# Performance work log

Measured on AMD Instinct MI355X. Metric: run time of the kernel, lower is better.

Reference implementation:

```python
import jax, jax.numpy as jnp
import numpy as np

C = 128        # dim_in = dim_out = dim_mid (exp_ratio=1.0)
HEADS = 4      # C // dim_head
DH = 32        # dim_head
WS = 7         # window_size
EPS = 1e-6
SCALE = DH ** -0.5


def bn3d(x, g, b):
    # BatchNorm3d forward (training-mode batch stats), eps=1e-6
    m = jnp.mean(x, axis=(0, 2, 3, 4), keepdims=True)
    v = jnp.mean((x - m) ** 2, axis=(0, 2, 3, 4), keepdims=True)
    xn = (x - m) * jax.lax.rsqrt(v + EPS)
    return xn * g.reshape(1, -1, 1, 1, 1) + b.reshape(1, -1, 1, 1, 1)


def conv1x1(x, w):
    # 1x1x1 conv, no bias: w is (out, in)
    return jnp.einsum('oi,bihwd->bohwd', w, x)


def setup_inputs() -> dict:
    key = jax.random.key(0)
    ks = jax.random.split(key, 6)
    x = jax.random.normal(ks[0], (4, C, 28, 28, 28), jnp.float32)
    g_in = jnp.ones((C,), jnp.float32)
    b_in = jnp.zeros((C,), jnp.float32)
    w_qk = jax.random.normal(ks[1], (2 * C, C), jnp.float32) * (C ** -0.5)
    w_v = jax.random.normal(ks[2], (C, C), jnp.float32) * (C ** -0.5)
    w_cl = jax.random.normal(ks[3], (C, C, 3, 3, 3), jnp.float32) * ((C * 27) ** -0.5)
    g_cl = jnp.ones((C,), jnp.float32)
    b_cl = jnp.zeros((C,), jnp.float32)
    w_proj = jax.random.normal(ks[4], (C, C), jnp.float32) * (C ** -0.5)
    return {"x": x, "g_in": g_in, "b_in": b_in, "w_qk": w_qk, "w_v": w_v,
            "w_cl": w_cl, "g_cl": g_cl, "b_cl": b_cl, "w_proj": w_proj}


def reference(x, g_in, b_in, w_qk, w_v, w_cl, g_cl, b_cl, w_proj):
    B, Cc, H, W, D = x.shape
    shortcut = x
    x = bn3d(x, g_in, b_in)

    # strided window partition: einops '(h1 n1)' => h1 (window) is the OUTER factor
    n1, n2, n3 = H // WS, W // WS, D // WS  # chosen divisible -> zero pad
    xw = x.reshape(B, Cc, WS, n1, WS, n2, WS, n3)
    xw = xw.transpose(0, 3, 5, 7, 1, 2, 4, 6).reshape(B * n1 * n2 * n3, Cc, WS, WS, WS)
    b = xw.shape[0]
    L = WS ** 3

    # qk: 1x1 conv -> split q,k -> (b, heads, L, dh)
    qk = conv1x1(xw, w_qk).reshape(b, 2, HEADS, DH, L)
    q = qk[:, 0].transpose(0, 1, 3, 2)       # b h L d
    k = qk[:, 1]                             # b h d L
    attn = jax.nn.softmax(jnp.einsum('bhld,bhdm->bhlm', q, k) * SCALE, axis=-1)

    # v: 1x1 conv + relu (attn_pre=False)
    v = jax.nn.relu(conv1x1(xw, w_v)).reshape(b, HEADS, DH, L)  # b h d L
    xs = jnp.einsum('bhlm,bhdm->bhld', attn, v)                 # b h L d
    xs = xs.transpose(0, 1, 3, 2).reshape(b, Cc, WS, WS, WS)

    # reverse window partition
    x = xs.reshape(B, n1, n2, n3, Cc, WS, WS, WS)
    x = x.transpose(0, 4, 5, 1, 6, 2, 7, 3).reshape(B, Cc, H, W, D)

    # local 3x3x3 conv + BN + SiLU, residual (has_skip inside iRMB branch)
    y = jax.lax.conv_general_dilated(
        x, w_cl, window_strides=(1, 1, 1),
        padding=[(1, 1), (1, 1), (1, 1)],
        dimension_numbers=('NCDHW', 'OIDHW', 'NCDHW'))
    y = jax.nn.silu(bn3d(y, g_cl, b_cl))
    x = x + y  # SE is Identity (se_ratio=0)

    x = conv1x1(x, w_proj)
    return shortcut + x
```

## Files before the change

### kernel.cpp

```cpp
#include <hip/hip_runtime.h>
#include <hip/hip_bf16.h>

#define C      128
#define SP     21952
#define PT     87808
#define LW     343
#define EPS_   1e-6f
#define SCALE_ 0.17677669529663687f

#define MISC_A   0
#define MISC_B   128
#define MISC_BQK 256
#define MISC_BV  512
#define MISC_SUM 640
#define MISC_SQ  768
#define MISC_A2  896
#define MISC_B2  1024
#define MISC_XS  1152
#define MISC_XQ  1280

typedef __attribute__((ext_vector_type(8))) short bf16x8;
typedef __attribute__((ext_vector_type(4))) float f32x4;

__device__ __forceinline__ float b2f(unsigned short u){
  return __uint_as_float(((unsigned int)u) << 16);
}
__device__ __forceinline__ unsigned short f2b(float f){
  unsigned int u = __float_as_uint(f);
  u += 0x7fffu + ((u >> 16) & 1u);
  return (unsigned short)(u >> 16);
}

__global__ __launch_bounds__(256) void k0_partial(const float* __restrict__ x,
                                                  float* __restrict__ misc){
  int c = blockIdx.x & 127, chunk = blockIdx.x >> 7;
  int bb = chunk >> 1, half = chunk & 1;
  const float4* p = reinterpret_cast<const float4*>(
      x + (size_t)(bb*C + c)*SP + half*10976);
  int t = threadIdx.x;
  float s = 0.f, ss = 0.f;
  for (int i = t; i < 2744; i += 256){
    float4 v = p[i];
    s  += v.x + v.y + v.z + v.w;
    ss += v.x*v.x + v.y*v.y + v.z*v.z + v.w*v.w;
  }
  #pragma unroll
  for (int off = 32; off > 0; off >>= 1){
    s  += __shfl_xor(s,  off);
    ss += __shfl_xor(ss, off);
  }
  __shared__ float red[8];
  int wid = t >> 6, lane = t & 63;
  if (lane == 0){ red[wid] = s; red[4+wid] = ss; }
  __syncthreads();
  if (t == 0){
    atomicAdd(&misc[MISC_XS + c], red[0]+red[1]+red[2]+red[3]);
    atomicAdd(&misc[MISC_XQ + c], red[4]+red[5]+red[6]+red[7]);
  }
}

__global__ void k1_bias(const float* __restrict__ wqk, const float* __restrict__ wvv,
                        const float* __restrict__ gin, const float* __restrict__ bin,
                        float* __restrict__ misc){
  __shared__ float bv[128];
  int t = threadIdx.x;
  {
    float mean = misc[MISC_XS + t] / (float)PT;
    float var  = misc[MISC_XQ + t] / (float)PT - mean*mean;
    float a = rsqrtf(var + EPS_) * gin[t];
    float bb = bin[t] - mean * a;
    bv[t] = bb;
    if (blockIdx.x == 0){ misc[MISC_A + t] = a; misc[MISC_B + t] = bb; }
  }
  __syncthreads();
  int o = blockIdx.x*128 + t;
  float acc = 0.f;
  if (o < 256){
    const float* wr = wqk + (size_t)o*128;
    for (int c = 0; c < 128; ++c) acc += wr[c]*bv[c];
    misc[MISC_BQK + o] = acc;
  } else {
    const float* wr = wvv + (size_t)(o-256)*128;
    for (int c = 0; c < 128; ++c) acc += wr[c]*bv[c];
    misc[MISC_BV + (o-256)] = acc;
  }
}

__global__ void k1w(const float* __restrict__ wqk, const float* __restrict__ wvv,
                    unsigned short* __restrict__ w2){
  int idx = blockIdx.x*256 + threadIdx.x;
  int o = idx >> 7;
  float w = (o < 256) ? wqk[idx] : wvv[idx - 32768];
  unsigned short h = f2b(w);
  w2[idx] = h;
  w2[49152 + idx] = f2b(w - b2f(h));
}

__global__ __launch_bounds__(256) void k2_qkv(const float* __restrict__ x,
        const unsigned short* __restrict__ w2, const float* __restrict__ misc,
        unsigned short* __restrict__ qg, unsigned short* __restrict__ kg,
        unsigned short* __restrict__ vg){
  __shared__ __align__(16) unsigned short xh[8192];
  __shared__ __align__(16) unsigned short xl[8192];
  __shared__ float ascale[128];
  __shared__ unsigned int posTab[64];
  int t = threadIdx.x;
  int P0 = blockIdx.x * 64;
  int b = P0 / SP, sp0 = P0 % SP;
  if (t < 128) ascale[t] = misc[MISC_A + t];
  if (t < 64){
    int sp = sp0 + t;
    int h_ = sp / 784, rem = sp % 784;
    int w_ = rem / 28, d_ = rem % 28;
    int w1 = h_ & 3, s1 = h_ >> 2;
    int w2i = w_ & 3, s2 = w_ >> 2;
    int w3 = d_ & 3, s3 = d_ >> 2;
    int bw = ((b*4 + w1)*4 + w2i)*4 + w3;
    int l  = (s1*7 + s2)*7 + s3;
    posTab[t] = (unsigned int)(bw*43904 + l*32);
  }
  __syncthreads();
  {
    int p = t & 63;
    int ob = t >> 6;
    const float* xb = x + (size_t)b*C*SP + sp0 + p;
    for (int it = 0; it < 4; ++it){
      int c0 = (ob + it*4) * 8;
      unsigned int ph[4], pl[4];
      #pragma unroll
      for (int j = 0; j < 4; ++j){
        float f0 = xb[(size_t)(c0 + 2*j)*SP]     * ascale[c0 + 2*j];
        float f1 = xb[(size_t)(c0 + 2*j + 1)*SP] * ascale[c0 + 2*j + 1];
        unsigned short h0 = f2b(f0), h1 = f2b(f1);
        unsigned short l0 = f2b(f0 - b2f(h0)), l1 = f2b(f1 - b2f(h1));
        ph[j] = (unsigned int)h0 | ((unsigned int)h1 << 16);
        pl[j] = (unsigned int)l0 | ((unsigned int)l1 << 16);
      }
      int byte = (p*256 + c0*2) ^ ((p & 7) << 4);
      *reinterpret_cast<uint4*>((char*)xh + byte) = make_uint4(ph[0],ph[1],ph[2],ph[3]);
      *reinterpret_cast<uint4*>((char*)xl + byte) = make_uint4(pl[0],pl[1],pl[2],pl[3]);
    }
  }
  __syncthreads();
  int wid = t >> 6, lane = t & 63;
  int g = lane >> 4, ln = lane & 15;
  int wstart = wid * 96;
  f32x4 acc[6][4];
  #pragma unroll
  for (int nt = 0; nt < 6; ++nt){
    float bv = misc[256 + wstart + nt*16 + ln];
    #pragma unroll
    for (int mt = 0; mt < 4; ++mt) acc[nt][mt] = (f32x4){bv,bv,bv,bv};
  }
  #pragma unroll 1
  for (int kk = 0; kk < 4; ++kk){
    bf16x8 ah[4], al[4];
    #pragma unroll
    for (int mt = 0; mt < 4; ++mt){
      int row = mt*16 + ln;
      int byte = (row*256 + kk*64 + g*16) ^ ((ln & 7) << 4);
      ah[mt] = *reinterpret_cast<const bf16x8*>((const char*)xh + byte);
      al[mt] = *reinterpret_cast<const bf16x8*>((const char*)xl + byte);
    }
    #pragma unroll
    for (int nt = 0; nt < 6; ++nt){
      int o = wstart + nt*16 + ln;
      const unsigned short* wp = w2 + (size_t)o*128 + kk*32 + g*8;
      bf16x8 whf = *reinterpret_cast<const bf16x8*>(wp);
      bf16x8 wlf = *reinterpret_cast<const bf16x8*>(wp + 49152);
      #pragma unroll
      for (int mt = 0; mt < 4; ++mt){
        acc[nt][mt] = __builtin_amdgcn_mfma_f32_16x16x32_bf16(ah[mt], whf, acc[nt][mt], 0, 0, 0);
        acc[nt][mt] = __builtin_amdgcn_mfma_f32_16x16x32_bf16(al[mt], whf, acc[nt][mt], 0, 0, 0);
        acc[nt][mt] = __builtin_amdgcn_mfma_f32_16x16x32_bf16(ah[mt], wlf, acc[nt][mt], 0, 0, 0);
      }
    }
  }
  unsigned int ptab[16];
  #pragma unroll
  for (int mt = 0; mt < 4; ++mt)
    #pragma unroll
    for (int r = 0; r < 4; ++r)
      ptab[mt*4+r] = posTab[mt*16 + g*4 + r];
  #pragma unroll
  for (int nt = 0; nt < 6; ++nt){
    int o = wstart + nt*16 + ln;
    bool isv = (o >= 256);
    int oo = o & 127;
    unsigned short* dst = ((o < 128) ? qg : (o < 256 ? kg : vg)) + (oo >> 5)*10976 + (oo & 31);
    #pragma unroll
    for (int mt = 0; mt < 4; ++mt){
      #pragma unroll
      for (int r = 0; r < 4; ++r){
        float v = acc[nt][mt][r];
        if (isv) v = fmaxf(v, 0.f);
        dst[ptab[mt*4+r]] = f2b(v);
      }
    }
  }
}

__global__ __launch_bounds__(256) void k3_attn(const unsigned short* __restrict__ qg,
        const unsigned short* __restrict__ kg, const unsigned short* __restrict__ vg,
        unsigned short* __restrict__ xatt){
  __shared__ __align__(16) unsigned short klds[352*32];
  __shared__ __align__(16) unsigned short vper[32*360];
  __shared__ __align__(16) unsigned short pbuf[4][640];
  int bh = blockIdx.x;
  int bw = bh >> 2, h = bh & 3;
  int t = threadIdx.x;
  int wid = t >> 6, lane = t & 63;
  int g = lane >> 4, ln = lane & 15;
  const unsigned short* kbase = kg + (size_t)bh*LW*32;
  const unsigned short* vbase = vg + (size_t)bh*LW*32;
  const unsigned short* qbase = qg + (size_t)bh*LW*32;
  {
    const uint4* src = reinterpret_cast<const uint4*>(kbase);
    uint4* dst = reinterpret_cast<uint4*>(klds);
    for (int i = t; i < 1372; i += 256) dst[i] = src[i];
    for (int i = t; i < 288; i += 256) klds[10976 + i] = 0;
  }
  for (int idx = t; idx < 10976; idx += 256){
    int m = idx >> 5, d = idx & 31;
    int km = m & 31;
    int pk = ((km & 15) << 1) | (km >> 4);
    vper[d*360 + ((m >> 5) << 5) + pk] = vbase[idx];
  }
  for (int i = t; i < 288; i += 256){
    int m = 343 + (i >> 5), d = i & 31;
    int km = m & 31;
    int pk = ((km & 15) << 1) | (km >> 4);
    vper[d*360 + 320 + pk] = 0;
  }
  __syncthreads();
  int w1 = (bw>>4)&3, w2 = (bw>>2)&3, w3 = bw&3, b = bw>>6;
  unsigned short* pb = pbuf[wid];
  const f32x4 zero4 = {0.f, 0.f, 0.f, 0.f};
  for (int rt = wid; rt < 22; rt += 4){
    int row0 = rt << 4;
    bf16x8 qf = *reinterpret_cast<const bf16x8*>(qbase + (size_t)(row0 + ln)*32 + g*8);
    f32x4 s[22];
    #pragma unroll
    for (int nt = 0; nt < 22; ++nt){
      bf16x8 kf = *reinterpret_cast<const bf16x8*>(&klds[(nt*16 + ln)*32 + g*8]);
      s[nt] = __builtin_amdgcn_mfma_f32_16x16x32_bf16(qf, kf, zero4, 0, 0, 0);
    }
    float mxs[4];
    #pragma unroll
    for (int q = 0; q < 4; ++q){
      float m0 = -1e30f;
      #pragma unroll
      for (int nt = 0; nt < 21; ++nt) m0 = fmaxf(m0, s[nt][q]);
      if (ln < 7) m0 = fmaxf(m0, s[21][q]);
      #pragma unroll
      for (int off = 8; off > 0; off >>= 1) m0 = fmaxf(m0, __shfl_xor(m0, off));
      mxs[q] = m0 * SCALE_;
    }
    f32x4 o0 = zero4, o1 = zero4;
    float sums[4] = {0.f, 0.f, 0.f, 0.f};
    #pragma unroll
    for (int c = 0; c < 11; ++c){
      #pragma unroll
      for (int q = 0; q < 4; ++q){
        float e0 = __expf(fmaf(s[2*c][q],   SCALE_, -mxs[q]));
        float e1 = (c*32 + 16 + ln < 343)
                 ? __expf(fmaf(s[2*c+1][q], SCALE_, -mxs[q])) : 0.f;
        sums[q] += e0 + e1;
        unsigned int pkd;
        asm volatile("v_cvt_pk_bf16_f32 %0, %1, %2" : "=v"(pkd) : "v"(e0), "v"(e1));
        *reinterpret_cast<unsigned int*>(&pb[(g*4+q)*40 + (ln<<1)]) = pkd;
      }
      asm volatile("s_waitcnt lgkmcnt(0)" ::: "memory");
      __builtin_amdgcn_sched_barrier(0);
      bf16x8 pa  = *reinterpret_cast<const bf16x8*>(&pb[ln*40 + g*8]);
      bf16x8 vb0 = *reinterpret_cast<const bf16x8*>(&vper[ln*360       + (c<<5) + g*8]);
      bf16x8 vb1 = *reinterpret_cast<const bf16x8*>(&vper[(16+ln)*360  + (c<<5) + g*8]);
      o0 = __builtin_amdgcn_mfma_f32_16x16x32_bf16(pa, vb0, o0, 0, 0, 0);
      o1 = __builtin_amdgcn_mfma_f32_16x16x32_bf16(pa, vb1, o1, 0, 0, 0);
    }
    float iss[4];
    #pragma unroll
    for (int q = 0; q < 4; ++q){
      float sq = sums[q];
      #pragma unroll
      for (int off = 8; off > 0; off >>= 1) sq += __shfl_xor(sq, off);
      iss[q] = 1.f / sq;
    }
    #pragma unroll
    for (int q = 0; q < 4; ++q){
      int l = row0 + g*4 + q;
      if (l < 343){
        int ss1 = l/49, ss2 = (l/7)%7, ss3 = l%7;
        int sp = (ss1*4+w1)*784 + (ss2*4+w2)*28 + (ss3*4+w3);
        size_t gaddr = ((size_t)b*SP + sp)*128 + h*32;
        xatt[gaddr + ln]      = f2b(o0[q]*iss[q]);
        xatt[gaddr + 16 + ln] = f2b(o1[q]*iss[q]);
      }
    }
  }
}

__global__ void k_wprep(const float* __restrict__ wcl, unsigned short* __restrict__ wbf){
  int f = blockIdx.x*256 + threadIdx.x;
  int j  = f & 7;
  int oc = (f >> 3) & 127;
  int kgr= (f >> 10) & 7;
  int sl = f >> 13;
  int h  = sl / 27, tap = sl % 27;
  int ic = h*64 + kgr*8 + j;
  wbf[f] = f2b(wcl[((size_t)oc*128 + ic)*27 + tap]);
}

__global__ void k6w(const float* __restrict__ wproj, unsigned short* __restrict__ w6){
  int idx = blockIdx.x*256 + threadIdx.x;
  float w = wproj[idx];
  unsigned short h = f2b(w);
  w6[idx] = h;
  w6[16384 + idx] = f2b(w - b2f(h));
}

__global__ __launch_bounds__(256) void k4_mfma(const unsigned short* __restrict__ xag,
        const unsigned short* __restrict__ wbf, unsigned short* __restrict__ yg){
  __shared__ __align__(16) unsigned short halo[8*216*8];
  __shared__ __align__(16) unsigned short wt[2][8192];
  int t = threadIdx.x, wid = t >> 6, lane = t & 63;
  int stile = blockIdx.x;
  int b = stile / 343, srem = stile % 343;
  int z0 = (srem/49)*4, y0 = ((srem/7)%7)*4, x0 = (srem%7)*4;
  int mhalf = wid & 1, ohalf = wid >> 1;
  int nn = lane & 15, quad = lane >> 4;
  int mA = mhalf*32 + nn;
  int mB = mA + 16;
  int hp0 = (mA>>4)*36 + ((mA>>2)&3)*6 + (mA&3);
  int hp1 = (mB>>4)*36 + ((mB>>2)&3)*6 + (mB&3);
  f32x4 acc[2][4] = {};

  #define WLOAD(s_, buf_) do { \
    const unsigned short* gs = wbf + (size_t)(s_)*8192 + (size_t)(wid*4*64 + lane)*8; \
    _Pragma("unroll") \
    for (int it = 0; it < 4; ++it){ \
      __builtin_amdgcn_global_load_lds( \
        (const __attribute__((address_space(1))) unsigned int*)(gs + it*512), \
        (__attribute__((address_space(3))) unsigned int*)(&wt[buf_][(wid*4+it)*512]), \
        16, 0, 0); \
    } \
  } while(0)

  int s = 0;
  WLOAD(0, 0);
  for (int h = 0; h < 2; ++h){
    for (int cidx = t; cidx < 1728; cidx += 256){
      int kgr = cidx / 216, pos = cidx % 216;
      int uz = pos / 36, r36 = pos % 36, uy = r36 / 6, ux = r36 % 6;
      int zz = z0 - 1 + uz, yy = y0 - 1 + uy, xx = x0 - 1 + ux;
      uint4 v = make_uint4(0u,0u,0u,0u);
      if (zz >= 0 && zz < 28 && yy >= 0 && yy < 28 && xx >= 0 && xx < 28)
        v = *reinterpret_cast<const uint4*>(
              &xag[(((size_t)b*SP) + zz*784 + yy*28 + xx)*128 + h*64 + kgr*8]);
      *reinterpret_cast<uint4*>(&halo[(size_t)cidx*8]) = v;
    }
    __syncthreads();
    for (int tap = 0; tap < 27; ++tap){
      if (s + 1 < 54) WLOAD(s + 1, (s + 1) & 1);
      const unsigned short* wc = wt[s & 1];
      int dz = tap / 9, r9 = tap % 9, dy = r9 / 3, dx = r9 % 3;
      int off = dz*36 + dy*6 + dx;
      #pragma unroll
      for (int ks = 0; ks < 2; ++ks){
        int ksel = ks*4 + quad;
        bf16x8 a0 = *reinterpret_cast<const bf16x8*>(&halo[(ksel*216 + hp0 + off)*8]);
        bf16x8 a1 = *reinterpret_cast<const bf16x8*>(&halo[(ksel*216 + hp1 + off)*8]);
        #pragma unroll
        for (int nt = 0; nt < 4; ++nt){
          bf16x8 bb = *reinterpret_cast<const bf16x8*>(&wc[(ksel*128 + ohalf*64 + nt*16 + nn)*8]);
          acc[0][nt] = __builtin_amdgcn_mfma_f32_16x16x32_bf16(a0, bb, acc[0][nt], 0, 0, 0);
          acc[1][nt] = __builtin_amdgcn_mfma_f32_16x16x32_bf16(a1, bb, acc[1][nt], 0, 0, 0);
        }
      }
      ++s;
      __syncthreads();
    }
  }
  #pragma unroll
  for (int mt = 0; mt < 2; ++mt){
    #pragma unroll
    for (int nt = 0; nt < 4; ++nt){
      #pragma unroll
      for (int r = 0; r < 4; ++r){
        int m = mhalf*32 + mt*16 + quad*4 + r;
        int oc = ohalf*64 + nt*16 + nn;
        int pos = (z0 + (m>>4))*784 + (y0 + ((m>>2)&3))*28 + (x0 + (m&3));
        yg[((size_t)b*SP + pos)*128 + oc] = f2b(acc[mt][nt][r]);
      }
    }
  }
  #undef WLOAD
}

__global__ void k5_ystats(const unsigned short* __restrict__ yg, float* __restrict__ misc){
  int t = threadIdx.x;
  float s = 0.f, ss = 0.f;
  size_t base = (size_t)blockIdx.x * 32768 + t;
  for (int k = 0; k < 128; ++k){
    float v = b2f(yg[base + (size_t)k*256]);
    s += v; ss += v*v;
  }
  __shared__ float rs[256], rq[256];
  rs[t] = s; rq[t] = ss;
  __syncthreads();
  if (t < 128){
    atomicAdd(&misc[MISC_SUM + t], rs[t] + rs[t+128]);
    atomicAdd(&misc[MISC_SQ  + t], rq[t] + rq[t+128]);
  }
}

__global__ void k5b_finstats(const float* __restrict__ gcl, const float* __restrict__ bcl,
                             float* __restrict__ misc){
  int c = threadIdx.x;
  float mean = misc[MISC_SUM+c] / (float)PT;
  float var  = misc[MISC_SQ +c] / (float)PT - mean*mean;
  float a = gcl[c] * rsqrtf(var + EPS_);
  misc[MISC_A2+c] = a;
  misc[MISC_B2+c] = bcl[c] - mean*a;
}

__global__ __launch_bounds__(256) void k6_final(const unsigned short* __restrict__ xag,
        const unsigned short* __restrict__ yg, const unsigned short* __restrict__ w6,
        const float* __restrict__ xin, const float* __restrict__ misc,
        float* __restrict__ out){
  __shared__ __align__(16) unsigned short xh[8192];
  __shared__ __align__(16) unsigned short xl[8192];
  __shared__ float a2s[128], b2s[128];
  int t = threadIdx.x;
  int P0 = blockIdx.x * 64;
  int b = P0 / SP, sp0 = P0 % SP;
  if (t < 128){ a2s[t] = misc[MISC_A2+t]; b2s[t] = misc[MISC_B2+t]; }
  __syncthreads();
  for (int idx = t; idx < 1024; idx += 256){
    int p = idx >> 4, c0 = (idx & 15) * 8;
    size_t gb = (size_t)(P0 + p)*128 + c0;
    uint4 yv4 = *reinterpret_cast<const uint4*>(yg + gb);
    uint4 xa4 = *reinterpret_cast<const uint4*>(xag + gb);
    unsigned int ph[4], pl[4];
    #pragma unroll
    for (int j = 0; j < 4; ++j){
      unsigned int uy = (&yv4.x)[j], ux = (&xa4.x)[j];
      int c = c0 + 2*j;
      float y0 = __uint_as_float(uy << 16)          * a2s[c]   + b2s[c];
      float y1 = __uint_as_float(uy & 0xffff0000u)  * a2s[c+1] + b2s[c+1];
      float v0 = __uint_as_float(ux << 16)         + y0 / (1.f + __expf(-y0));
      float v1 = __uint_as_float(ux & 0xffff0000u) + y1 / (1.f + __expf(-y1));
      unsigned short h0 = f2b(v0), h1 = f2b(v1);
      unsigned short l0 = f2b(v0 - b2f(h0)), l1 = f2b(v1 - b2f(h1));
      ph[j] = (unsigned int)h0 | ((unsigned int)h1 << 16);
      pl[j] = (unsigned int)l0 | ((unsigned int)l1 << 16);
    }
    int byte = (p*256 + c0*2) ^ ((p & 7) << 4);
    *reinterpret_cast<uint4*>((char*)xh + byte) = make_uint4(ph[0],ph[1],ph[2],ph[3]);
    *reinterpret_cast<uint4*>((char*)xl + byte) = make_uint4(pl[0],pl[1],pl[2],pl[3]);
  }
  __syncthreads();
  int wid = t >> 6, lane = t & 63;
  int g = lane >> 4, ln = lane & 15;
  f32x4 acc[2][4] = {};
  #pragma unroll 1
  for (int kk = 0; kk < 4; ++kk){
    bf16x8 bh[4], bl[4];
    #pragma unroll
    for (int pt = 0; pt < 4; ++pt){
      int row = pt*16 + ln;
      int byte = (row*256 + kk*64 + g*16) ^ ((ln & 7) << 4);
      bh[pt] = *reinterpret_cast<const bf16x8*>((const char*)xh + byte);
      bl[pt] = *reinterpret_cast<const bf16x8*>((const char*)xl + byte);
    }
    #pragma unroll
    for (int ot = 0; ot < 2; ++ot){
      int o = wid*32 + ot*16 + ln;
      const unsigned short* wp = w6 + (size_t)o*128 + kk*32 + g*8;
      bf16x8 wh = *reinterpret_cast<const bf16x8*>(wp);
      bf16x8 wl = *reinterpret_cast<const bf16x8*>(wp + 16384);
      #pragma unroll
      for (int pt = 0; pt < 4; ++pt){
        acc[ot][pt] = __builtin_amdgcn_mfma_f32_16x16x32_bf16(wh, bh[pt], acc[ot][pt], 0, 0, 0);
        acc[ot][pt] = __builtin_amdgcn_mfma_f32_16x16x32_bf16(wl, bh[pt], acc[ot][pt], 0, 0, 0);
        acc[ot][pt] = __builtin_amdgcn_mfma_f32_16x16x32_bf16(wh, bl[pt], acc[ot][pt], 0, 0, 0);
      }
    }
  }
  #pragma unroll
  for (int ot = 0; ot < 2; ++ot){
    #pragma unroll
    for (int r = 0; r < 4; ++r){
      int o = wid*32 + ot*16 + g*4 + r;
      size_t gbase = ((size_t)b*128 + o)*SP + sp0;
      #pragma unroll
      for (int pt = 0; pt < 4; ++pt){
        size_t gaddr = gbase + pt*16 + ln;
        out[gaddr] = xin[gaddr] + acc[ot][pt][r];
      }
    }
  }
}

extern "C" void kernel_launch(void* const* d_in, const int* in_sizes, int n_in,
                              void* d_out, int out_size, void* d_ws, size_t ws_size,
                              hipStream_t stream){
  const float* x      = (const float*)d_in[0];
  const float* g_in   = (const float*)d_in[1];
  const float* b_in   = (const float*)d_in[2];
  const float* w_qk   = (const float*)d_in[3];
  const float* w_v    = (const float*)d_in[4];
  const float* w_cl   = (const float*)d_in[5];
  const float* g_cl   = (const float*)d_in[6];
  const float* b_cl   = (const float*)d_in[7];
  const float* w_proj = (const float*)d_in[8];
  float* out = (float*)d_out;

  char* ws = (char*)d_ws;
  unsigned short* qg  = (unsigned short*)ws;
  unsigned short* kgp = qg  + 11239424;
  unsigned short* vg  = kgp + 11239424;
  unsigned short* xag = vg  + 11239424;
  unsigned short* yg  = xag + 11239424;
  float* misc = (float*)(ws + (size_t)5*22478848);
  unsigned short* wbf = qg;
  unsigned short* w6  = qg + 524288;
  unsigned short* w2  = yg;

  hipMemsetAsync(misc + MISC_SUM, 0, 768*sizeof(float), stream);
  k0_partial  <<<1024, 256, 0, stream>>>(x, misc);
  k1_bias     <<<3, 128, 0, stream>>>(w_qk, w_v, g_in, b_in, misc);
  k1w         <<<192, 256, 0, stream>>>(w_qk, w_v, w2);
  k2_qkv      <<<1372, 256, 0, stream>>>(x, w2, misc, qg, kgp, vg);
  k3_attn     <<<1024, 256, 0, stream>>>(qg, kgp, vg, xag);
  k_wprep     <<<1728, 256, 0, stream>>>(w_cl, wbf);
  k6w         <<<64, 256, 0, stream>>>(w_proj, w6);
  k4_mfma     <<<1372, 256, 0, stream>>>(xag, wbf, yg);
  k5_ystats   <<<343, 256, 0, stream>>>(yg, misc);
  k5b_finstats<<<1, 128, 0, stream>>>(g_cl, b_cl, misc);
  k6_final    <<<1372, 256, 0, stream>>>(xag, yg, w6, x, misc, out);
}
```

Measured before the change: 422.0 us.

## Register-stream conv weights in 2-wave MFMA tile and vectorize BN stats reduction

The 3x3x3 conv kernel drops the LDS double-buffered weight tile and per-tap barriers. It now runs 128 threads per block, each wave computing all 64 spatial rows for half the output channels, with B fragments prefetched from global memory into registers in a ping-pong pattern. This removes the LDS weight traffic and 54 block syncs per tile, at the cost of more registers (64 accumulators and 16 B fragments) and fewer waves per block. The y-statistics kernel now reads 16-byte vectors across channels and reduces them with shuffles and LDS atomics instead of scalar strided loads.

```diff
diff --git a/kernel.cpp b/kernel.cpp
--- a/kernel.cpp
+++ b/kernel.cpp
@@ -319,37 +319,54 @@
   w6[16384 + idx] = f2b(w - b2f(h));
 }
 
-__global__ __launch_bounds__(256) void k4_mfma(const unsigned short* __restrict__ xag,
+__global__ __launch_bounds__(128) void k4_mfma(const unsigned short* __restrict__ xag,
         const unsigned short* __restrict__ wbf, unsigned short* __restrict__ yg){
   __shared__ __align__(16) unsigned short halo[8*216*8];
-  __shared__ __align__(16) unsigned short wt[2][8192];
   int t = threadIdx.x, wid = t >> 6, lane = t & 63;
+  int g = lane >> 4, ln = lane & 15;
   int stile = blockIdx.x;
   int b = stile / 343, srem = stile % 343;
   int z0 = (srem/49)*4, y0 = ((srem/7)%7)*4, x0 = (srem%7)*4;
-  int mhalf = wid & 1, ohalf = wid >> 1;
-  int nn = lane & 15, quad = lane >> 4;
-  int mA = mhalf*32 + nn;
-  int mB = mA + 16;
-  int hp0 = (mA>>4)*36 + ((mA>>2)&3)*6 + (mA&3);
-  int hp1 = (mB>>4)*36 + ((mB>>2)&3)*6 + (mB&3);
-  f32x4 acc[2][4] = {};
-
-  #define WLOAD(s_, buf_) do { \
-    const unsigned short* gs = wbf + (size_t)(s_)*8192 + (size_t)(wid*4*64 + lane)*8; \
+  int ohalf = wid;
+  int hp = (ln>>2)*6 + (ln&3);
+  f32x4 acc[4][4] = {};
+  const unsigned short* wb0 = wbf + (size_t)(g*1024 + ohalf*512 + ln*8);
+  bf16x8 b0[8], b1[8];
+
+  #define BLOADX(dst_, s_) do { \
+    const unsigned short* wp_ = wb0 + (size_t)(s_)*8192; \
     _Pragma("unroll") \
-    for (int it = 0; it < 4; ++it){ \
-      __builtin_amdgcn_global_load_lds( \
-        (const __attribute__((address_space(1))) unsigned int*)(gs + it*512), \
-        (__attribute__((address_space(3))) unsigned int*)(&wt[buf_][(wid*4+it)*512]), \
-        16, 0, 0); \
-    } \
+    for (int ks_ = 0; ks_ < 2; ++ks_) \
+      _Pragma("unroll") \
+      for (int nt_ = 0; nt_ < 4; ++nt_) \
+        dst_[ks_*4+nt_] = *reinterpret_cast<const bf16x8*>(wp_ + ks_*4096 + nt_*128); \
   } while(0)
 
+  #define COMPUTE(tap_, buf_) do { \
+    int dz_ = (tap_)/9, r9_ = (tap_)%9, dy_ = r9_/3, dx_ = r9_%3; \
+    int off_ = dz_*36 + dy_*6 + dx_; \
+    bf16x8 af_[2][4]; \
+    _Pragma("unroll") \
+    for (int ks_ = 0; ks_ < 2; ++ks_) \
+      _Pragma("unroll") \
+      for (int mt_ = 0; mt_ < 4; ++mt_) \
+        af_[ks_][mt_] = *reinterpret_cast<const bf16x8*>( \
+            &halo[((ks_*4 + g)*216 + mt_*36 + hp + off_)*8]); \
+    _Pragma("unroll") \
+    for (int nt_ = 0; nt_ < 4; ++nt_) \
+      _Pragma("unroll") \
+      for (int ks_ = 0; ks_ < 2; ++ks_) \
+        _Pragma("unroll") \
+        for (int mt_ = 0; mt_ < 4; ++mt_) \
+          acc[nt_][mt_] = __builtin_amdgcn_mfma_f32_16x16x32_bf16( \
+              af_[ks_][mt_], buf_[ks_*4+nt_], acc[nt_][mt_], 0, 0, 0); \
+  } while(0)
+
   int s = 0;
-  WLOAD(0, 0);
+  BLOADX(b0, 0);
   for (int h = 0; h < 2; ++h){
-    for (int cidx = t; cidx < 1728; cidx += 256){
+    if (h) __syncthreads();
+    for (int cidx = t; cidx < 1728; cidx += 128){
       int kgr = cidx / 216, pos = cidx % 216;
       int uz = pos / 36, r36 = pos % 36, uy = r36 / 6, ux = r36 % 6;
       int zz = z0 - 1 + uz, yy = y0 - 1 + uy, xx = x0 - 1 + ux;
@@ -360,57 +377,71 @@
       *reinterpret_cast<uint4*>(&halo[(size_t)cidx*8]) = v;
     }
     __syncthreads();
-    for (int tap = 0; tap < 27; ++tap){
-      if (s + 1 < 54) WLOAD(s + 1, (s + 1) & 1);
-      const unsigned short* wc = wt[s & 1];
-      int dz = tap / 9, r9 = tap % 9, dy = r9 / 3, dx = r9 % 3;
-      int off = dz*36 + dy*6 + dx;
-      #pragma unroll
-      for (int ks = 0; ks < 2; ++ks){
-        int ksel = ks*4 + quad;
-        bf16x8 a0 = *reinterpret_cast<const bf16x8*>(&halo[(ksel*216 + hp0 + off)*8]);
-        bf16x8 a1 = *reinterpret_cast<const bf16x8*>(&halo[(ksel*216 + hp1 + off)*8]);
-        #pragma unroll
-        for (int nt = 0; nt < 4; ++nt){
-          bf16x8 bb = *reinterpret_cast<const bf16x8*>(&wc[(ksel*128 + ohalf*64 + nt*16 + nn)*8]);
-          acc[0][nt] = __builtin_amdgcn_mfma_f32_16x16x32_bf16(a0, bb, acc[0][nt], 0, 0, 0);
-          acc[1][nt] = __builtin_amdgcn_mfma_f32_16x16x32_bf16(a1, bb, acc[1][nt], 0, 0, 0);
-        }
-      }
-      ++s;
-      __syncthreads();
-    }
-  }
-  #pragma unroll
-  for (int mt = 0; mt < 2; ++mt){
-    #pragma unroll
-    for (int nt = 0; nt < 4; ++nt){
+    for (int tp = 0; tp < 26; tp += 2){
+      BLOADX(b1, s+1);
+      COMPUTE(tp, b0);
+      BLOADX(b0, s+2);
+      COMPUTE(tp+1, b1);
+      s += 2;
+    }
+    COMPUTE(26, b0);
+    ++s;
+    if (s < 54) BLOADX(b0, s);
+  }
+  #pragma unroll
+  for (int nt = 0; nt < 4; ++nt){
+    int oc = ohalf*64 + nt*16 + ln;
+    #pragma unroll
+    for (int mt = 0; mt < 4; ++mt){
       #pragma unroll
       for (int r = 0; r < 4; ++r){
-        int m = mhalf*32 + mt*16 + quad*4 + r;
-        int oc = ohalf*64 + nt*16 + nn;
-        int pos = (z0 + (m>>4))*784 + (y0 + ((m>>2)&3))*28 + (x0 + (m&3));
-        yg[((size_t)b*SP + pos)*128 + oc] = f2b(acc[mt][nt][r]);
-      }
-    }
-  }
-  #undef WLOAD
-}
-
-__global__ void k5_ystats(const unsigned short* __restrict__ yg, float* __restrict__ misc){
+        int pos = (z0 + mt)*784 + (y0 + g)*28 + (x0 + r);
+        yg[((size_t)b*SP + pos)*128 + oc] = f2b(acc[nt][mt][r]);
+      }
+    }
+  }
+  #undef BLOADX
+  #undef COMPUTE
+}
+
+__global__ __launch_bounds__(256) void k5_ystats(const unsigned short* __restrict__ yg,
+                                                 float* __restrict__ misc){
   int t = threadIdx.x;
-  float s = 0.f, ss = 0.f;
-  size_t base = (size_t)blockIdx.x * 32768 + t;
-  for (int k = 0; k < 128; ++k){
-    float v = b2f(yg[base + (size_t)k*256]);
-    s += v; ss += v*v;
-  }
-  __shared__ float rs[256], rq[256];
-  rs[t] = s; rq[t] = ss;
+  int c8 = t & 15;
+  int pr = t >> 4;
+  float s[8] = {0,0,0,0,0,0,0,0}, q[8] = {0,0,0,0,0,0,0,0};
+  size_t base = (size_t)blockIdx.x * 256;
+  for (int i = 0; i < 16; ++i){
+    size_t pos = base + i*16 + pr;
+    uint4 v = *reinterpret_cast<const uint4*>(yg + pos*128 + c8*8);
+    #pragma unroll
+    for (int j = 0; j < 4; ++j){
+      unsigned int u = (&v.x)[j];
+      float f0 = __uint_as_float(u << 16);
+      float f1 = __uint_as_float(u & 0xffff0000u);
+      s[2*j]   += f0; q[2*j]   += f0*f0;
+      s[2*j+1] += f1; q[2*j+1] += f1*f1;
+    }
+  }
+  #pragma unroll
+  for (int j = 0; j < 8; ++j){
+    s[j] += __shfl_xor(s[j], 16); q[j] += __shfl_xor(q[j], 16);
+    s[j] += __shfl_xor(s[j], 32); q[j] += __shfl_xor(q[j], 32);
+  }
+  __shared__ float rs[128], rq[128];
+  if (t < 128){ rs[t] = 0.f; rq[t] = 0.f; }
+  __syncthreads();
+  if ((t & 48) == 0){
+    #pragma unroll
+    for (int j = 0; j < 8; ++j){
+      atomicAdd(&rs[c8*8+j], s[j]);
+      atomicAdd(&rq[c8*8+j], q[j]);
+    }
+  }
   __syncthreads();
   if (t < 128){
-    atomicAdd(&misc[MISC_SUM + t], rs[t] + rs[t+128]);
-    atomicAdd(&misc[MISC_SQ  + t], rq[t] + rq[t+128]);
+    atomicAdd(&misc[MISC_SUM + t], rs[t]);
+    atomicAdd(&misc[MISC_SQ  + t], rq[t]);
   }
 }
 
@@ -535,7 +566,7 @@
   k3_attn     <<<1024, 256, 0, stream>>>(qg, kgp, vg, xag);
   k_wprep     <<<1728, 256, 0, stream>>>(w_cl, wbf);
   k6w         <<<64, 256, 0, stream>>>(w_proj, w6);
-  k4_mfma     <<<1372, 256, 0, stream>>>(xag, wbf, yg);
+  k4_mfma     <<<1372, 128, 0, stream>>>(xag, wbf, yg);
   k5_ystats   <<<343, 256, 0, stream>>>(yg, misc);
   k5b_finstats<<<1, 128, 0, stream>>>(g_cl, b_cl, misc);
   k6_final    <<<1372, 256, 0, stream>>>(xag, yg, w6, x, misc, out);
```

Result: faster. 391.7 us (-7.2%).
